# Kernel optimization log

Measured on AMD Instinct MI355X. Metric: run time of the kernel, lower is better.

Reference implementation:

```python
import jax, jax.numpy as jnp
import numpy as np

D_MODEL = 1024
N_HEAD = 16


def setup_inputs() -> dict:
    key = jax.random.key(0)
    ks = jax.random.split(key, 11)
    B, S, D = 2, 2048, D_MODEL
    s = 1.0 / np.sqrt(D)
    inp = {
        "q": jax.random.normal(ks[0], (B, S, D), jnp.float32),
        "k": jax.random.normal(ks[1], (B, S, D), jnp.float32),
        "v": jax.random.normal(ks[2], (B, S, D), jnp.float32),
        "Wq": jax.random.normal(ks[3], (D, D), jnp.float32) * s,
        "bq": jnp.zeros((D,), jnp.float32),
        "Wk": jax.random.normal(ks[4], (D, D), jnp.float32) * s,
        "bk": jnp.zeros((D,), jnp.float32),
        "Wv": jax.random.normal(ks[5], (D, D), jnp.float32) * s,
        "bv": jnp.zeros((D,), jnp.float32),
        "Wo": jax.random.normal(ks[6], (D, D), jnp.float32) * s,
        "bo": jnp.zeros((D,), jnp.float32),
    }
    return inp


def _split(x, n_head):
    B, S, D = x.shape
    return x.reshape(B, S, n_head, D // n_head).transpose(0, 2, 1, 3)  # [B,H,S,dh]


def reference(q, k, v, Wq, bq, Wk, bk, Wv, bv, Wo, bo):
    # Linear projections (torch Linear: x @ W.T + b), add_noise=False path
    qh = _split(q @ Wq.T + bq, N_HEAD)
    kh = _split(k @ Wk.T + bk, N_HEAD)
    vh = _split(v @ Wv.T + bv, N_HEAD)
    d_tensor = qh.shape[-1]
    # score = q @ k^T / sqrt(d_tensor); mask=None
    score = jnp.einsum('bhqd,bhkd->bhqk', qh, kh) / jnp.sqrt(jnp.float32(d_tensor))
    attn = jax.nn.softmax(score, axis=-1)
    out = jnp.einsum('bhqk,bhkd->bhqd', attn, vh)
    B, H, S, dh = out.shape
    out = out.transpose(0, 2, 1, 3).reshape(B, S, H * dh)
    return out @ Wo.T + bo
```

## Files before the change

kernel.cpp:

```cpp
#include <hip/hip_runtime.h>
#include <stdint.h>

typedef unsigned short u16;
typedef short bfx8 __attribute__((ext_vector_type(8)));
typedef float fx4 __attribute__((ext_vector_type(4)));

#define B_  2
#define S_  2048
#define D_  1024
#define H_  16
#define DH  64
#define K_  1024
#define M_ROWS 4096
#define QSCALE 0.18033688011112042f


__device__ __forceinline__ u16 f2bf(float x) {
  union { float f; uint32_t u; } c; c.f = x;
  uint32_t r = (c.u + 0x7FFFu + ((c.u >> 16) & 1u)) >> 16;
  return (u16)r;
}

__device__ __forceinline__ fx4 mfma16(bfx8 a, bfx8 b, fx4 c) {
  return __builtin_amdgcn_mfma_f32_16x16x32_bf16(a, b, c, 0, 0, 0);
}

typedef const __attribute__((address_space(1))) void as1_cvoid;
typedef __attribute__((address_space(3))) void as3_void;

__device__ __forceinline__ void stage16(const void* g, void* l) {
  __builtin_amdgcn_global_load_lds((as1_cvoid*)g, (as3_void*)l, 16, 0, 0);
}

__device__ __forceinline__ bfx8 lds_frag(const u16* base, int row, int kelem) {
  int off = (row << 7) + (kelem << 1);
  off ^= (row & 7) << 4;
  return *reinterpret_cast<const bfx8*>(reinterpret_cast<const char*>(base) + off);
}

__device__ __forceinline__ uint32_t cvt_pk_bf16(float lo, float hi) {
  uint32_t r;
  asm("v_cvt_pk_bf16_f32 %0, %1, %2" : "=v"(r) : "v"(lo), "v"(hi));
  return r;
}

__device__ __forceinline__ float exp2_raw(float x) {
  float r;
  asm("v_exp_f32 %0, %1" : "=v"(r) : "v"(x));
  return r;
}


__global__ __launch_bounds__(256) void convert_kernel(
    const float* __restrict__ q, const float* __restrict__ k, const float* __restrict__ v,
    const float* __restrict__ wq, const float* __restrict__ wk, const float* __restrict__ wv,
    const float* __restrict__ wo,
    u16* __restrict__ qb, u16* __restrict__ kb, u16* __restrict__ vb,
    u16* __restrict__ wqb, u16* __restrict__ wkb, u16* __restrict__ wvb,
    u16* __restrict__ wob) {
  const float* s; u16* d; int n8;
  switch (blockIdx.y) {
    case 0: s = q;  d = qb;  n8 = (M_ROWS * D_) / 8; break;
    case 1: s = k;  d = kb;  n8 = (M_ROWS * D_) / 8; break;
    case 2: s = v;  d = vb;  n8 = (M_ROWS * D_) / 8; break;
    case 3: s = wq; d = wqb; n8 = (D_ * D_) / 8; break;
    case 4: s = wk; d = wkb; n8 = (D_ * D_) / 8; break;
    case 5: s = wv; d = wvb; n8 = (D_ * D_) / 8; break;
    default: s = wo; d = wob; n8 = (D_ * D_) / 8; break;
  }
  int idx = blockIdx.x * blockDim.x + threadIdx.x;
  if (idx >= n8) return;
  const float4* sp = reinterpret_cast<const float4*>(s) + (size_t)idx * 2;
  float4 a = sp[0], b = sp[1];
  bfx8 r;
  r[0] = (short)f2bf(a.x); r[1] = (short)f2bf(a.y);
  r[2] = (short)f2bf(a.z); r[3] = (short)f2bf(a.w);
  r[4] = (short)f2bf(b.x); r[5] = (short)f2bf(b.y);
  r[6] = (short)f2bf(b.z); r[7] = (short)f2bf(b.w);
  *reinterpret_cast<bfx8*>(d + (size_t)idx * 8) = r;
}


__device__ __forceinline__ void g128_stage(const u16* __restrict__ A,
                                           const u16* __restrict__ Bt,
                                           int m0, int n0, int k0,
                                           u16* Ad, u16* Bd,
                                           int w, int l8, int c8) {
  #pragma unroll
  for (int i = 0; i < 4; ++i) {
    int j = (w << 2) + i;
    int row = (j << 3) + l8;
    int sc = c8 ^ (row & 7);
    stage16(A + (size_t)(m0 + row) * K_ + k0 + (sc << 3), Ad + (j << 9));
    stage16(Bt + (size_t)(n0 + row) * K_ + k0 + (sc << 3), Bd + (j << 9));
  }
}

__device__ __forceinline__ void gemm128_core(const u16* __restrict__ A,
                                             const u16* __restrict__ Bt,
                                             int m0, int n0,
                                             u16 (*Al)[128 * 64], u16 (*Bl)[128 * 64],
                                             fx4 (&acc)[4][4]) {
  const int lane = threadIdx.x & 63;
  const int w = threadIdx.x >> 6;
  const int l8 = lane >> 3, c8 = lane & 7;
  const int fr = lane & 15, fk = (lane >> 4) << 3;
  const int wr = (w >> 1) << 6, wc = (w & 1) << 6;

  g128_stage(A, Bt, m0, n0, 0, Al[0], Bl[0], w, l8, c8);
  __syncthreads();
  for (int t = 0; t < K_ / 64; ++t) {
    const int cur = t & 1;
    if (t + 1 < K_ / 64)
      g128_stage(A, Bt, m0, n0, (t + 1) * 64, Al[cur ^ 1], Bl[cur ^ 1], w, l8, c8);
    __builtin_amdgcn_s_setprio(1);
    #pragma unroll
    for (int kb = 0; kb < 2; ++kb) {
      bfx8 af[4], bf[4];
      #pragma unroll
      for (int rb = 0; rb < 4; ++rb)
        af[rb] = lds_frag(Al[cur], wr + rb * 16 + fr, kb * 32 + fk);
      #pragma unroll
      for (int cb = 0; cb < 4; ++cb)
        bf[cb] = lds_frag(Bl[cur], wc + cb * 16 + fr, kb * 32 + fk);
      #pragma unroll
      for (int rb = 0; rb < 4; ++rb)
        #pragma unroll
        for (int cb = 0; cb < 4; ++cb)
          acc[rb][cb] = mfma16(af[rb], bf[cb], acc[rb][cb]);
    }
    __builtin_amdgcn_s_setprio(0);
    __syncthreads();
  }
}


__global__ __launch_bounds__(256, 2) void proj_gemm(
    const u16* __restrict__ qb, const u16* __restrict__ kb, const u16* __restrict__ vb,
    const u16* __restrict__ wqb, const u16* __restrict__ wkb, const u16* __restrict__ wvb,
    const float* __restrict__ bq, const float* __restrict__ bk, const float* __restrict__ bv,
    u16* __restrict__ Qh, u16* __restrict__ Kh, u16* __restrict__ VT) {
  __shared__ alignas(16) u16 Al[2][128 * 64];
  __shared__ alignas(16) u16 Bl[2][128 * 64];
  int bid = (blockIdx.x & 7) * 96 + (blockIdx.x >> 3);
  int z = bid >> 8;
  int t = bid & 255;
  const u16 *A, *Bt; const float* bias;
  if (z == 0)      { A = qb;  Bt = wqb; bias = bq; }
  else if (z == 1) { A = kb;  Bt = wkb; bias = bk; }
  else             { A = wvb; Bt = vb;  bias = bv; }
  int m0, n0;
  if (z < 2) { m0 = (t >> 3) << 7; n0 = (t & 7) << 7; }
  else       { m0 = (t >> 5) << 7; n0 = (t & 31) << 7; }

  fx4 acc[4][4];
  #pragma unroll
  for (int i = 0; i < 4; ++i)
    #pragma unroll
    for (int j = 0; j < 4; ++j) acc[i][j] = (fx4){0.f, 0.f, 0.f, 0.f};

  gemm128_core(A, Bt, m0, n0, Al, Bl, acc);

  const int lane = threadIdx.x & 63;
  const int w = threadIdx.x >> 6;
  const int wr = (w >> 1) << 6, wc = (w & 1) << 6;
  const int fr = lane & 15;
  const int rq = (lane >> 4) << 2;

  if (z < 2) {
    u16* O = (z == 0) ? Qh : Kh;
    float scale = (z == 0) ? QSCALE : 1.0f;
    #pragma unroll
    for (int cb = 0; cb < 4; ++cb) {
      int n = n0 + wc + cb * 16 + fr;
      float bn = bias[n];
      int h = n >> 6, dd = n & 63;
      #pragma unroll
      for (int rb = 0; rb < 4; ++rb) {
        #pragma unroll
        for (int r = 0; r < 4; ++r) {
          int m = m0 + wr + rb * 16 + rq + r;
          int b = m >> 11, srow = m & 2047;
          O[((size_t)((b * H_ + h) * S_ + srow) << 6) + dd] =
              f2bf((acc[rb][cb][r] + bn) * scale);
        }
      }
    }
  } else {
    #pragma unroll
    for (int rb = 0; rb < 4; ++rb) {
      #pragma unroll
      for (int r = 0; r < 4; ++r) {
        int m = m0 + wr + rb * 16 + rq + r;
        float bm = bias[m];
        int h = m >> 6, dd = m & 63;
        #pragma unroll
        for (int cb = 0; cb < 4; ++cb) {
          int n = n0 + wc + cb * 16 + fr;
          int b = n >> 11, srow = n & 2047;
          VT[(size_t)((b * H_ + h) * DH + dd) * S_ + srow] =
              f2bf(acc[rb][cb][r] + bm);
        }
      }
    }
  }
}


__global__ __launch_bounds__(256, 2) void attn_kernel(
    const u16* __restrict__ Qh, const u16* __restrict__ Kh,
    const u16* __restrict__ VT, u16* __restrict__ AO) {
  __shared__ alignas(16) u16 Klds[2][64 * 64];
  __shared__ alignas(16) u16 Vlds[2][64 * 64];

  const int blk = ((blockIdx.x & 7) << 6) + (blockIdx.x >> 3);
  const int bh = blk >> 4;
  const int qt = blk & 15;
  const int tid = threadIdx.x;
  const int lane = tid & 63;
  const int w = tid >> 6;
  const int q0 = (qt << 7) + (w << 5);
  const int c = lane & 15;
  const int g = lane >> 4;
  const int l8 = lane >> 3;
  const int c8 = lane & 7;
  const int sc = c8 ^ l8;
  const size_t base = (size_t)bh * (S_ * DH);
  const u16* Qp = Qh + base;
  const int b = bh >> 4, h = bh & 15;

  bfx8 qf[2][2];
  #pragma unroll
  for (int rb = 0; rb < 2; ++rb)
    #pragma unroll
    for (int kbi = 0; kbi < 2; ++kbi)
      qf[rb][kbi] = *reinterpret_cast<const bfx8*>(
          Qp + (size_t)(q0 + rb * 16 + c) * DH + kbi * 32 + (g << 3));

  bfx8 ones;
  #pragma unroll
  for (int i = 0; i < 8; ++i) ones[i] = (short)0x3F80;

  fx4 acc[2][4];
  fx4 accl[2];
  #pragma unroll
  for (int rb = 0; rb < 2; ++rb) {
    accl[rb] = (fx4){0.f, 0.f, 0.f, 0.f};
    #pragma unroll
    for (int db = 0; db < 4; ++db) acc[rb][db] = (fx4){0.f, 0.f, 0.f, 0.f};
  }

  const int colA = ((g ^ (c & 3)) << 4);
  const int f6 = (c & 4) << 4;
  const int laneK = c * 128 + colA;
  const char* kb_0[2] = { (const char*)Klds[0] + laneK + f6,
                          (const char*)Klds[0] + laneK + (f6 ^ 64) };
  const char* kb_1[2] = { (const char*)Klds[1] + laneK + f6,
                          (const char*)Klds[1] + laneK + (f6 ^ 64) };
  const char* vb_0[2] = { (const char*)Vlds[0] + laneK + f6,
                          (const char*)Vlds[0] + laneK + (f6 ^ 64) };
  const char* vb_1[2] = { (const char*)Vlds[1] + laneK + f6,
                          (const char*)Vlds[1] + laneK + (f6 ^ 64) };

  const u16* kS0 = Kh + base + (size_t)((w << 4) + l8) * DH + (sc << 3);
  const u16* kS1 = kS0 + 8 * DH;
  const u16* vS0 = VT + base + (size_t)((w << 4) + l8) * S_ + (sc << 3);
  const u16* vS1 = vS0 + 8 * S_;
  u16* kD_0[2] = { &Klds[0][(2 * w) << 9], &Klds[0][(2 * w + 1) << 9] };
  u16* kD_1[2] = { &Klds[1][(2 * w) << 9], &Klds[1][(2 * w + 1) << 9] };
  u16* vD_0[2] = { &Vlds[0][(2 * w) << 9], &Vlds[0][(2 * w + 1) << 9] };
  u16* vD_1[2] = { &Vlds[1][(2 * w) << 9], &Vlds[1][(2 * w + 1) << 9] };

#define STAGEB(bi)                                                            \
  do {                                                                        \
    stage16(kS0, kD_##bi[0]); stage16(kS1, kD_##bi[1]);                       \
    stage16(vS0, vD_##bi[0]); stage16(vS1, vD_##bi[1]);                       \
    kS0 += 64 * DH; kS1 += 64 * DH; vS0 += 64; vS1 += 64;                     \
  } while (0)

#define COMPUTE(bi)                                                           \
  do {                                                                        \
    fx4 sf[2][4];                                                             \
    _Pragma("unroll") for (int rb = 0; rb < 2; ++rb)                          \
      _Pragma("unroll") for (int cb = 0; cb < 4; ++cb)                        \
        sf[rb][cb] = (fx4){0.f, 0.f, 0.f, 0.f};                               \
    __builtin_amdgcn_s_setprio(1);                                            \
    _Pragma("unroll") for (int kbi = 0; kbi < 2; ++kbi) {                     \
      bfx8 kf[4];                                                             \
      _Pragma("unroll") for (int cb = 0; cb < 4; ++cb)                        \
        kf[cb] = *reinterpret_cast<const bfx8*>(kb_##bi[kbi] + cb * 2048);    \
      _Pragma("unroll") for (int rb = 0; rb < 2; ++rb)                        \
        _Pragma("unroll") for (int cb = 0; cb < 4; ++cb)                      \
          sf[rb][cb] = mfma16(kf[cb], qf[rb][kbi], sf[rb][cb]);               \
    }                                                                         \
    __builtin_amdgcn_s_setprio(0);                                            \
    uint32_t E[2][2][2][2];                                                   \
    _Pragma("unroll") for (int rb = 0; rb < 2; ++rb) {                        \
      _Pragma("unroll") for (int cb = 0; cb < 4; ++cb)                        \
        _Pragma("unroll") for (int r = 0; r < 4; ++r)                         \
          sf[rb][cb][r] = exp2_raw(sf[rb][cb][r]);                            \
      _Pragma("unroll") for (int cb = 0; cb < 4; ++cb)                        \
        _Pragma("unroll") for (int hh = 0; hh < 2; ++hh)                      \
          E[rb][cb >> 1][cb & 1][hh] =                                        \
              cvt_pk_bf16(sf[rb][cb][2 * hh], sf[rb][cb][2 * hh + 1]);        \
      _Pragma("unroll") for (int r2 = 0; r2 < 2; ++r2)                        \
        _Pragma("unroll") for (int r0 = 0; r0 < 2; ++r0) {                    \
          asm("v_permlane32_swap_b32 %0, %1"                                  \
              : "+v"(E[rb][r2][0][r0]), "+v"(E[rb][r2][1][r0]));              \
          asm("v_permlane16_swap_b32 %0, %1"                                  \
              : "+v"(E[rb][r2][0][r0]), "+v"(E[rb][r2][1][r0]));              \
        }                                                                     \
    }                                                                         \
    __builtin_amdgcn_s_setprio(1);                                            \
    _Pragma("unroll") for (int kbi = 0; kbi < 2; ++kbi) {                     \
      bfx8 vf[4];                                                             \
      _Pragma("unroll") for (int db = 0; db < 4; ++db)                        \
        vf[db] = *reinterpret_cast<const bfx8*>(vb_##bi[kbi] + db * 2048);    \
      _Pragma("unroll") for (int rb = 0; rb < 2; ++rb) {                      \
        union { uint32_t wd[4]; bfx8 v; } pu;                                 \
        pu.wd[0] = E[rb][kbi][0][0]; pu.wd[1] = E[rb][kbi][0][1];             \
        pu.wd[2] = E[rb][kbi][1][0]; pu.wd[3] = E[rb][kbi][1][1];             \
        _Pragma("unroll") for (int db = 0; db < 4; ++db)                      \
          acc[rb][db] = mfma16(pu.v, vf[db], acc[rb][db]);                    \
        accl[rb] = mfma16(pu.v, ones, accl[rb]);                              \
      }                                                                       \
    }                                                                         \
    __builtin_amdgcn_s_setprio(0);                                            \
  } while (0)

  STAGEB(0);
  __syncthreads();

  for (int kv = 0; kv < S_; kv += 128) {
    STAGEB(1);
    COMPUTE(0);
    __syncthreads();
    if (kv + 128 < S_) STAGEB(0);
    COMPUTE(1);
    __syncthreads();
  }
#undef STAGEB
#undef COMPUTE

  #pragma unroll
  for (int rb = 0; rb < 2; ++rb) {
    float invb[4];
    #pragma unroll
    for (int r = 0; r < 4; ++r) invb[r] = 1.0f / accl[rb][r];
    #pragma unroll
    for (int db = 0; db < 4; ++db)
      #pragma unroll
      for (int r = 0; r < 4; ++r) {
        int qrow = q0 + rb * 16 + (g << 2) + r;
        AO[(size_t)(b * S_ + qrow) * D_ + h * DH + db * 16 + c] =
            f2bf(acc[rb][db][r] * invb[r]);
      }
  }
}


__global__ __launch_bounds__(256, 2) void out_gemm(
    const u16* __restrict__ AO, const u16* __restrict__ wob,
    const float* __restrict__ bo, float* __restrict__ out) {
  __shared__ alignas(16) u16 Al[2][128 * 64];
  __shared__ alignas(16) u16 Bl[2][128 * 64];
  int t = (blockIdx.x & 7) * 32 + (blockIdx.x >> 3);
  int m0 = (t >> 3) << 7, n0 = (t & 7) << 7;
  fx4 acc[4][4];
  #pragma unroll
  for (int i = 0; i < 4; ++i)
    #pragma unroll
    for (int j = 0; j < 4; ++j) acc[i][j] = (fx4){0.f, 0.f, 0.f, 0.f};
  gemm128_core(AO, wob, m0, n0, Al, Bl, acc);
  const int lane = threadIdx.x & 63;
  const int w = threadIdx.x >> 6;
  const int wr = (w >> 1) << 6, wc = (w & 1) << 6;
  #pragma unroll
  for (int cb = 0; cb < 4; ++cb) {
    int n = n0 + wc + cb * 16 + (lane & 15);
    float bn = bo[n];
    #pragma unroll
    for (int rb = 0; rb < 4; ++rb)
      #pragma unroll
      for (int r = 0; r < 4; ++r) {
        int m = m0 + wr + rb * 16 + ((lane >> 4) << 2) + r;
        out[(size_t)m * D_ + n] = acc[rb][cb][r] + bn;
      }
  }
}


extern "C" void kernel_launch(void* const* d_in, const int* in_sizes, int n_in,
                              void* d_out, int out_size, void* d_ws, size_t ws_size,
                              hipStream_t stream) {
  (void)in_sizes; (void)n_in; (void)out_size;
  const size_t MB = 1024 * 1024;
  if (ws_size < 56 * MB) return;

  const float* q  = (const float*)d_in[0];
  const float* k  = (const float*)d_in[1];
  const float* v  = (const float*)d_in[2];
  const float* Wq = (const float*)d_in[3];
  const float* bq = (const float*)d_in[4];
  const float* Wk = (const float*)d_in[5];
  const float* bk = (const float*)d_in[6];
  const float* Wv = (const float*)d_in[7];
  const float* bv = (const float*)d_in[8];
  const float* Wo = (const float*)d_in[9];
  const float* bo = (const float*)d_in[10];
  float* out = (float*)d_out;

  char* ws = (char*)d_ws;
  u16* qb  = (u16*)(ws);
  u16* kb  = (u16*)(ws + 8 * MB);
  u16* vb  = (u16*)(ws + 16 * MB);
  u16* wqb = (u16*)(ws + 24 * MB);
  u16* wkb = (u16*)(ws + 26 * MB);
  u16* wvb = (u16*)(ws + 28 * MB);
  u16* wob = (u16*)(ws + 30 * MB);
  u16* Qh  = (u16*)(ws + 32 * MB);
  u16* Kh  = (u16*)(ws + 40 * MB);
  u16* VT  = (u16*)(ws + 48 * MB);
  u16* AO  = qb;

  convert_kernel<<<dim3(2048, 7), 256, 0, stream>>>(q, k, v, Wq, Wk, Wv, Wo,
                                                    qb, kb, vb, wqb, wkb, wvb, wob);
  proj_gemm<<<768, 256, 0, stream>>>(qb, kb, vb, wqb, wkb, wvb, bq, bk, bv, Qh, Kh, VT);
  attn_kernel<<<512, 256, 0, stream>>>(Qh, Kh, VT, AO);
  out_gemm<<<256, 256, 0, stream>>>(AO, wob, bo, out);
}
```

Measured before the change: 214.5 us.

## Fuse fp32-to-bf16 conversion into GEMM tile loading and drop convert kernel

Removes the separate conversion kernel. The projection and output GEMMs now load fp32 inputs and weights straight from global memory into registers, convert them to bf16 with packed converts, and write them into swizzled LDS double buffers. This saves one launch and a full write-then-reread of bf16 copies. In exchange, each GEMM tile reloads twice as many bytes of fp32 data, and weights are converted again by every block that reads them. Register-staged prefetch replaces the async LDS staging for those operands.

Measured after the change: 232.4 us. +8.3%, slower.

```diff
diff --git a/kernel.cpp b/kernel.cpp
--- a/kernel.cpp
+++ b/kernel.cpp
@@ -50,94 +50,58 @@
   return r;
 }
 
-
-__global__ __launch_bounds__(256) void convert_kernel(
-    const float* __restrict__ q, const float* __restrict__ k, const float* __restrict__ v,
-    const float* __restrict__ wq, const float* __restrict__ wk, const float* __restrict__ wv,
-    const float* __restrict__ wo,
-    u16* __restrict__ qb, u16* __restrict__ kb, u16* __restrict__ vb,
-    u16* __restrict__ wqb, u16* __restrict__ wkb, u16* __restrict__ wvb,
-    u16* __restrict__ wob) {
-  const float* s; u16* d; int n8;
-  switch (blockIdx.y) {
-    case 0: s = q;  d = qb;  n8 = (M_ROWS * D_) / 8; break;
-    case 1: s = k;  d = kb;  n8 = (M_ROWS * D_) / 8; break;
-    case 2: s = v;  d = vb;  n8 = (M_ROWS * D_) / 8; break;
-    case 3: s = wq; d = wqb; n8 = (D_ * D_) / 8; break;
-    case 4: s = wk; d = wkb; n8 = (D_ * D_) / 8; break;
-    case 5: s = wv; d = wvb; n8 = (D_ * D_) / 8; break;
-    default: s = wo; d = wob; n8 = (D_ * D_) / 8; break;
-  }
-  int idx = blockIdx.x * blockDim.x + threadIdx.x;
-  if (idx >= n8) return;
-  const float4* sp = reinterpret_cast<const float4*>(s) + (size_t)idx * 2;
-  float4 a = sp[0], b = sp[1];
-  bfx8 r;
-  r[0] = (short)f2bf(a.x); r[1] = (short)f2bf(a.y);
-  r[2] = (short)f2bf(a.z); r[3] = (short)f2bf(a.w);
-  r[4] = (short)f2bf(b.x); r[5] = (short)f2bf(b.y);
-  r[6] = (short)f2bf(b.z); r[7] = (short)f2bf(b.w);
-  *reinterpret_cast<bfx8*>(d + (size_t)idx * 8) = r;
-}
-
-
-__device__ __forceinline__ void g128_stage(const u16* __restrict__ A,
-                                           const u16* __restrict__ Bt,
-                                           int m0, int n0, int k0,
-                                           u16* Ad, u16* Bd,
-                                           int w, int l8, int c8) {
+struct f32x8 { float4 a, b; };
+__device__ __forceinline__ f32x8 ld8(const float* p) {
+  const float4* p4 = reinterpret_cast<const float4*>(p);
+  f32x8 r; r.a = p4[0]; r.b = p4[1]; return r;
+}
+__device__ __forceinline__ void wr8(u16* d, f32x8 v) {
+  union { uint32_t w[4]; bfx8 x; } u;
+  u.w[0] = cvt_pk_bf16(v.a.x, v.a.y);
+  u.w[1] = cvt_pk_bf16(v.a.z, v.a.w);
+  u.w[2] = cvt_pk_bf16(v.b.x, v.b.y);
+  u.w[3] = cvt_pk_bf16(v.b.z, v.b.w);
+  *reinterpret_cast<bfx8*>(d) = u.x;
+}
+
+__device__ __forceinline__ void g128_stageA(const u16* __restrict__ A,
+                                            int m0, int k0, u16* Ad,
+                                            int w, int l8, int c8) {
   #pragma unroll
   for (int i = 0; i < 4; ++i) {
     int j = (w << 2) + i;
     int row = (j << 3) + l8;
     int sc = c8 ^ (row & 7);
     stage16(A + (size_t)(m0 + row) * K_ + k0 + (sc << 3), Ad + (j << 9));
-    stage16(Bt + (size_t)(n0 + row) * K_ + k0 + (sc << 3), Bd + (j << 9));
-  }
-}
-
-__device__ __forceinline__ void gemm128_core(const u16* __restrict__ A,
-                                             const u16* __restrict__ Bt,
-                                             int m0, int n0,
-                                             u16 (*Al)[128 * 64], u16 (*Bl)[128 * 64],
-                                             fx4 (&acc)[4][4]) {
-  const int lane = threadIdx.x & 63;
-  const int w = threadIdx.x >> 6;
-  const int l8 = lane >> 3, c8 = lane & 7;
-  const int fr = lane & 15, fk = (lane >> 4) << 3;
-  const int wr = (w >> 1) << 6, wc = (w & 1) << 6;
-
-  g128_stage(A, Bt, m0, n0, 0, Al[0], Bl[0], w, l8, c8);
-  __syncthreads();
-  for (int t = 0; t < K_ / 64; ++t) {
-    const int cur = t & 1;
-    if (t + 1 < K_ / 64)
-      g128_stage(A, Bt, m0, n0, (t + 1) * 64, Al[cur ^ 1], Bl[cur ^ 1], w, l8, c8);
-    __builtin_amdgcn_s_setprio(1);
-    #pragma unroll
-    for (int kb = 0; kb < 2; ++kb) {
-      bfx8 af[4], bf[4];
-      #pragma unroll
-      for (int rb = 0; rb < 4; ++rb)
-        af[rb] = lds_frag(Al[cur], wr + rb * 16 + fr, kb * 32 + fk);
+  }
+}
+
+__device__ __forceinline__ void mfma_block(const u16* Ac, const u16* Bc,
+                                           int wr, int wc, int fr, int fk,
+                                           fx4 (&acc)[4][4]) {
+  __builtin_amdgcn_s_setprio(1);
+  #pragma unroll
+  for (int kb = 0; kb < 2; ++kb) {
+    bfx8 af[4], bf[4];
+    #pragma unroll
+    for (int rb = 0; rb < 4; ++rb)
+      af[rb] = lds_frag(Ac, wr + rb * 16 + fr, kb * 32 + fk);
+    #pragma unroll
+    for (int cb = 0; cb < 4; ++cb)
+      bf[cb] = lds_frag(Bc, wc + cb * 16 + fr, kb * 32 + fk);
+    #pragma unroll
+    for (int rb = 0; rb < 4; ++rb)
       #pragma unroll
       for (int cb = 0; cb < 4; ++cb)
-        bf[cb] = lds_frag(Bl[cur], wc + cb * 16 + fr, kb * 32 + fk);
-      #pragma unroll
-      for (int rb = 0; rb < 4; ++rb)
-        #pragma unroll
-        for (int cb = 0; cb < 4; ++cb)
-          acc[rb][cb] = mfma16(af[rb], bf[cb], acc[rb][cb]);
-    }
-    __builtin_amdgcn_s_setprio(0);
-    __syncthreads();
-  }
+        acc[rb][cb] = mfma16(af[rb], bf[cb], acc[rb][cb]);
+  }
+  __builtin_amdgcn_s_setprio(0);
 }
 
 
 __global__ __launch_bounds__(256, 2) void proj_gemm(
-    const u16* __restrict__ qb, const u16* __restrict__ kb, const u16* __restrict__ vb,
-    const u16* __restrict__ wqb, const u16* __restrict__ wkb, const u16* __restrict__ wvb,
+    const float* __restrict__ q, const float* __restrict__ k, const float* __restrict__ v,
+    const float* __restrict__ Wq, const float* __restrict__ Wk, const float* __restrict__ Wv,
     const float* __restrict__ bq, const float* __restrict__ bk, const float* __restrict__ bv,
     u16* __restrict__ Qh, u16* __restrict__ Kh, u16* __restrict__ VT) {
   __shared__ alignas(16) u16 Al[2][128 * 64];
@@ -145,28 +109,67 @@
   int bid = (blockIdx.x & 7) * 96 + (blockIdx.x >> 3);
   int z = bid >> 8;
   int t = bid & 255;
-  const u16 *A, *Bt; const float* bias;
-  if (z == 0)      { A = qb;  Bt = wqb; bias = bq; }
-  else if (z == 1) { A = kb;  Bt = wkb; bias = bk; }
-  else             { A = wvb; Bt = vb;  bias = bv; }
+  const float *A, *Bt; const float* bias;
+  if (z == 0)      { A = q;  Bt = Wq; bias = bq; }
+  else if (z == 1) { A = k;  Bt = Wk; bias = bk; }
+  else             { A = Wv; Bt = v;  bias = bv; }
   int m0, n0;
   if (z < 2) { m0 = (t >> 3) << 7; n0 = (t & 7) << 7; }
   else       { m0 = (t >> 5) << 7; n0 = (t & 31) << 7; }
 
-  fx4 acc[4][4];
-  #pragma unroll
-  for (int i = 0; i < 4; ++i)
-    #pragma unroll
-    for (int j = 0; j < 4; ++j) acc[i][j] = (fx4){0.f, 0.f, 0.f, 0.f};
-
-  gemm128_core(A, Bt, m0, n0, Al, Bl, acc);
-
   const int lane = threadIdx.x & 63;
   const int w = threadIdx.x >> 6;
+  const int l8 = lane >> 3, c8 = lane & 7;
+  const int fr = lane & 15, fk = (lane >> 4) << 3;
   const int wr = (w >> 1) << 6, wc = (w & 1) << 6;
-  const int fr = lane & 15;
+
+  const float* As[4]; const float* Bs[4]; int doff[4];
+  #pragma unroll
+  for (int i = 0; i < 4; ++i) {
+    int j = (w << 2) + i, row = (j << 3) + l8, sc = c8 ^ (row & 7);
+    As[i] = A + (size_t)(m0 + row) * K_ + (sc << 3);
+    Bs[i] = Bt + (size_t)(n0 + row) * K_ + (sc << 3);
+    doff[i] = (j << 9) + (lane << 3);
+  }
+
+  fx4 acc[4][4];
+  #pragma unroll
+  for (int i = 0; i < 4; ++i)
+    #pragma unroll
+    for (int j = 0; j < 4; ++j) acc[i][j] = (fx4){0.f, 0.f, 0.f, 0.f};
+
+  f32x8 ra[4], rb[4];
+  #pragma unroll
+  for (int i = 0; i < 4; ++i) {
+    ra[i] = ld8(As[i]); rb[i] = ld8(Bs[i]);
+    As[i] += 64; Bs[i] += 64;
+  }
+  #pragma unroll
+  for (int i = 0; i < 4; ++i) {
+    wr8(&Al[0][doff[i]], ra[i]); wr8(&Bl[0][doff[i]], rb[i]);
+  }
+  __syncthreads();
+
+  for (int tt = 0; tt < 16; ++tt) {
+    const int cur = tt & 1;
+    if (tt < 15) {
+      #pragma unroll
+      for (int i = 0; i < 4; ++i) {
+        ra[i] = ld8(As[i]); rb[i] = ld8(Bs[i]);
+        As[i] += 64; Bs[i] += 64;
+      }
+    }
+    mfma_block(Al[cur], Bl[cur], wr, wc, fr, fk, acc);
+    if (tt < 15) {
+      #pragma unroll
+      for (int i = 0; i < 4; ++i) {
+        wr8(&Al[cur ^ 1][doff[i]], ra[i]); wr8(&Bl[cur ^ 1][doff[i]], rb[i]);
+      }
+    }
+    __syncthreads();
+  }
+
   const int rq = (lane >> 4) << 2;
-
   if (z < 2) {
     u16* O = (z == 0) ? Qh : Kh;
     float scale = (z == 0) ? QSCALE : 1.0f;
@@ -176,22 +179,22 @@
       float bn = bias[n];
       int h = n >> 6, dd = n & 63;
       #pragma unroll
-      for (int rb = 0; rb < 4; ++rb) {
+      for (int rb_ = 0; rb_ < 4; ++rb_) {
         #pragma unroll
         for (int r = 0; r < 4; ++r) {
-          int m = m0 + wr + rb * 16 + rq + r;
+          int m = m0 + wr + rb_ * 16 + rq + r;
           int b = m >> 11, srow = m & 2047;
           O[((size_t)((b * H_ + h) * S_ + srow) << 6) + dd] =
-              f2bf((acc[rb][cb][r] + bn) * scale);
+              f2bf((acc[rb_][cb][r] + bn) * scale);
         }
       }
     }
   } else {
     #pragma unroll
-    for (int rb = 0; rb < 4; ++rb) {
+    for (int rb_ = 0; rb_ < 4; ++rb_) {
       #pragma unroll
       for (int r = 0; r < 4; ++r) {
-        int m = m0 + wr + rb * 16 + rq + r;
+        int m = m0 + wr + rb_ * 16 + rq + r;
         float bm = bias[m];
         int h = m >> 6, dd = m & 63;
         #pragma unroll
@@ -199,7 +202,7 @@
           int n = n0 + wc + cb * 16 + fr;
           int b = n >> 11, srow = n & 2047;
           VT[(size_t)((b * H_ + h) * DH + dd) * S_ + srow] =
-              f2bf(acc[rb][cb][r] + bm);
+              f2bf(acc[rb_][cb][r] + bm);
         }
       }
     }
@@ -360,31 +363,66 @@
 
 
 __global__ __launch_bounds__(256, 2) void out_gemm(
-    const u16* __restrict__ AO, const u16* __restrict__ wob,
+    const u16* __restrict__ AO, const float* __restrict__ Wo,
     const float* __restrict__ bo, float* __restrict__ out) {
   __shared__ alignas(16) u16 Al[2][128 * 64];
   __shared__ alignas(16) u16 Bl[2][128 * 64];
   int t = (blockIdx.x & 7) * 32 + (blockIdx.x >> 3);
   int m0 = (t >> 3) << 7, n0 = (t & 7) << 7;
-  fx4 acc[4][4];
-  #pragma unroll
-  for (int i = 0; i < 4; ++i)
-    #pragma unroll
-    for (int j = 0; j < 4; ++j) acc[i][j] = (fx4){0.f, 0.f, 0.f, 0.f};
-  gemm128_core(AO, wob, m0, n0, Al, Bl, acc);
+
   const int lane = threadIdx.x & 63;
   const int w = threadIdx.x >> 6;
+  const int l8 = lane >> 3, c8 = lane & 7;
+  const int fr = lane & 15, fk = (lane >> 4) << 3;
   const int wr = (w >> 1) << 6, wc = (w & 1) << 6;
+
+  const float* Bs[4]; int doff[4];
+  #pragma unroll
+  for (int i = 0; i < 4; ++i) {
+    int j = (w << 2) + i, row = (j << 3) + l8, sc = c8 ^ (row & 7);
+    Bs[i] = Wo + (size_t)(n0 + row) * K_ + (sc << 3);
+    doff[i] = (j << 9) + (lane << 3);
+  }
+
+  fx4 acc[4][4];
+  #pragma unroll
+  for (int i = 0; i < 4; ++i)
+    #pragma unroll
+    for (int j = 0; j < 4; ++j) acc[i][j] = (fx4){0.f, 0.f, 0.f, 0.f};
+
+  f32x8 rb[4];
+  #pragma unroll
+  for (int i = 0; i < 4; ++i) { rb[i] = ld8(Bs[i]); Bs[i] += 64; }
+  #pragma unroll
+  for (int i = 0; i < 4; ++i) wr8(&Bl[0][doff[i]], rb[i]);
+  g128_stageA(AO, m0, 0, Al[0], w, l8, c8);
+  __syncthreads();
+
+  for (int tt = 0; tt < 16; ++tt) {
+    const int cur = tt & 1;
+    if (tt < 15) {
+      g128_stageA(AO, m0, (tt + 1) * 64, Al[cur ^ 1], w, l8, c8);
+      #pragma unroll
+      for (int i = 0; i < 4; ++i) { rb[i] = ld8(Bs[i]); Bs[i] += 64; }
+    }
+    mfma_block(Al[cur], Bl[cur], wr, wc, fr, fk, acc);
+    if (tt < 15) {
+      #pragma unroll
+      for (int i = 0; i < 4; ++i) wr8(&Bl[cur ^ 1][doff[i]], rb[i]);
+    }
+    __syncthreads();
+  }
+
   #pragma unroll
   for (int cb = 0; cb < 4; ++cb) {
-    int n = n0 + wc + cb * 16 + (lane & 15);
+    int n = n0 + wc + cb * 16 + fr;
     float bn = bo[n];
     #pragma unroll
-    for (int rb = 0; rb < 4; ++rb)
+    for (int rb_ = 0; rb_ < 4; ++rb_)
       #pragma unroll
       for (int r = 0; r < 4; ++r) {
-        int m = m0 + wr + rb * 16 + ((lane >> 4) << 2) + r;
-        out[(size_t)m * D_ + n] = acc[rb][cb][r] + bn;
+        int m = m0 + wr + rb_ * 16 + ((lane >> 4) << 2) + r;
+        out[(size_t)m * D_ + n] = acc[rb_][cb][r] + bn;
       }
   }
 }
@@ -395,7 +433,7 @@
                               hipStream_t stream) {
   (void)in_sizes; (void)n_in; (void)out_size;
   const size_t MB = 1024 * 1024;
-  if (ws_size < 56 * MB) return;
+  if (ws_size < 32 * MB) return;
 
   const float* q  = (const float*)d_in[0];
   const float* k  = (const float*)d_in[1];
@@ -411,21 +449,12 @@
   float* out = (float*)d_out;
 
   char* ws = (char*)d_ws;
-  u16* qb  = (u16*)(ws);
-  u16* kb  = (u16*)(ws + 8 * MB);
-  u16* vb  = (u16*)(ws + 16 * MB);
-  u16* wqb = (u16*)(ws + 24 * MB);
-  u16* wkb = (u16*)(ws + 26 * MB);
-  u16* wvb = (u16*)(ws + 28 * MB);
-  u16* wob = (u16*)(ws + 30 * MB);
-  u16* Qh  = (u16*)(ws + 32 * MB);
-  u16* Kh  = (u16*)(ws + 40 * MB);
-  u16* VT  = (u16*)(ws + 48 * MB);
-  u16* AO  = qb;
-
-  convert_kernel<<<dim3(2048, 7), 256, 0, stream>>>(q, k, v, Wq, Wk, Wv, Wo,
-                                                    qb, kb, vb, wqb, wkb, wvb, wob);
-  proj_gemm<<<768, 256, 0, stream>>>(qb, kb, vb, wqb, wkb, wvb, bq, bk, bv, Qh, Kh, VT);
+  u16* Qh = (u16*)(ws);
+  u16* Kh = (u16*)(ws + 8 * MB);
+  u16* VT = (u16*)(ws + 16 * MB);
+  u16* AO = (u16*)(ws + 24 * MB);
+
+  proj_gemm<<<768, 256, 0, stream>>>(q, k, v, Wq, Wk, Wv, bq, bk, bv, Qh, Kh, VT);
   attn_kernel<<<512, 256, 0, stream>>>(Qh, Kh, VT, AO);
-  out_gemm<<<256, 256, 0, stream>>>(AO, wob, bo, out);
-}
+  out_gemm<<<256, 256, 0, stream>>>(AO, Wo, bo, out);
+}
```

## Split attention KV range across two wave groups and halve out-GEMM tile width

Applied to the files above, without the earlier changes.

The attention kernel now launches 512 threads per block. Two groups of four waves each process half of the key/value sequence with their own LDS double buffers, and the partial accumulators and row sums are merged through shared memory before normalisation. This doubles the wave count per query tile to hide latency and improve occupancy, at the cost of a final LDS reduction and a larger shared-memory footprint. The output GEMM switches to 128x64 tiles with 512 blocks and an inline staging loop, giving better fill across CUs with less B reuse per block.

New measurement: 209.7 us. 1.02x faster.

```diff
diff --git a/kernel.cpp b/kernel.cpp
--- a/kernel.cpp
+++ b/kernel.cpp
@@ -207,11 +207,10 @@
 }
 
 
-__global__ __launch_bounds__(256, 2) void attn_kernel(
+__global__ __launch_bounds__(512, 4) void attn_kernel(
     const u16* __restrict__ Qh, const u16* __restrict__ Kh,
     const u16* __restrict__ VT, u16* __restrict__ AO) {
-  __shared__ alignas(16) u16 Klds[2][64 * 64];
-  __shared__ alignas(16) u16 Vlds[2][64 * 64];
+  __shared__ alignas(16) u16 SH[2][2][2][64 * 64];
 
   const int blk = ((blockIdx.x & 7) << 6) + (blockIdx.x >> 3);
   const int bh = blk >> 4;
@@ -219,7 +218,9 @@
   const int tid = threadIdx.x;
   const int lane = tid & 63;
   const int w = tid >> 6;
-  const int q0 = (qt << 7) + (w << 5);
+  const int grp = w >> 2;
+  const int wl = w & 3;
+  const int q0 = (qt << 7) + (wl << 5);
   const int c = lane & 15;
   const int g = lane >> 4;
   const int l8 = lane >> 3;
@@ -253,23 +254,23 @@
   const int colA = ((g ^ (c & 3)) << 4);
   const int f6 = (c & 4) << 4;
   const int laneK = c * 128 + colA;
-  const char* kb_0[2] = { (const char*)Klds[0] + laneK + f6,
-                          (const char*)Klds[0] + laneK + (f6 ^ 64) };
-  const char* kb_1[2] = { (const char*)Klds[1] + laneK + f6,
-                          (const char*)Klds[1] + laneK + (f6 ^ 64) };
-  const char* vb_0[2] = { (const char*)Vlds[0] + laneK + f6,
-                          (const char*)Vlds[0] + laneK + (f6 ^ 64) };
-  const char* vb_1[2] = { (const char*)Vlds[1] + laneK + f6,
-                          (const char*)Vlds[1] + laneK + (f6 ^ 64) };
-
-  const u16* kS0 = Kh + base + (size_t)((w << 4) + l8) * DH + (sc << 3);
+  const char* kb_0[2] = { (const char*)&SH[grp][0][0][0] + laneK + f6,
+                          (const char*)&SH[grp][0][0][0] + laneK + (f6 ^ 64) };
+  const char* kb_1[2] = { (const char*)&SH[grp][1][0][0] + laneK + f6,
+                          (const char*)&SH[grp][1][0][0] + laneK + (f6 ^ 64) };
+  const char* vb_0[2] = { (const char*)&SH[grp][0][1][0] + laneK + f6,
+                          (const char*)&SH[grp][0][1][0] + laneK + (f6 ^ 64) };
+  const char* vb_1[2] = { (const char*)&SH[grp][1][1][0] + laneK + f6,
+                          (const char*)&SH[grp][1][1][0] + laneK + (f6 ^ 64) };
+
+  const u16* kS0 = Kh + base + (size_t)(grp * 1024 + (wl << 4) + l8) * DH + (sc << 3);
   const u16* kS1 = kS0 + 8 * DH;
-  const u16* vS0 = VT + base + (size_t)((w << 4) + l8) * S_ + (sc << 3);
+  const u16* vS0 = VT + base + (size_t)((wl << 4) + l8) * S_ + grp * 1024 + (sc << 3);
   const u16* vS1 = vS0 + 8 * S_;
-  u16* kD_0[2] = { &Klds[0][(2 * w) << 9], &Klds[0][(2 * w + 1) << 9] };
-  u16* kD_1[2] = { &Klds[1][(2 * w) << 9], &Klds[1][(2 * w + 1) << 9] };
-  u16* vD_0[2] = { &Vlds[0][(2 * w) << 9], &Vlds[0][(2 * w + 1) << 9] };
-  u16* vD_1[2] = { &Vlds[1][(2 * w) << 9], &Vlds[1][(2 * w + 1) << 9] };
+  u16* kD_0[2] = { &SH[grp][0][0][(2 * wl) << 9], &SH[grp][0][0][(2 * wl + 1) << 9] };
+  u16* kD_1[2] = { &SH[grp][1][0][(2 * wl) << 9], &SH[grp][1][0][(2 * wl + 1) << 9] };
+  u16* vD_0[2] = { &SH[grp][0][1][(2 * wl) << 9], &SH[grp][0][1][(2 * wl + 1) << 9] };
+  u16* vD_1[2] = { &SH[grp][1][1][(2 * wl) << 9], &SH[grp][1][1][(2 * wl + 1) << 9] };
 
 #define STAGEB(bi)                                                            \
   do {                                                                        \
@@ -331,30 +332,59 @@
   STAGEB(0);
   __syncthreads();
 
-  for (int kv = 0; kv < S_; kv += 128) {
+  for (int t = 0; t < 16; t += 2) {
     STAGEB(1);
     COMPUTE(0);
     __syncthreads();
-    if (kv + 128 < S_) STAGEB(0);
+    if (t + 2 < 16) STAGEB(0);
     COMPUTE(1);
     __syncthreads();
   }
 #undef STAGEB
 #undef COMPUTE
 
-  #pragma unroll
-  for (int rb = 0; rb < 2; ++rb) {
-    float invb[4];
-    #pragma unroll
-    for (int r = 0; r < 4; ++r) invb[r] = 1.0f / accl[rb][r];
-    #pragma unroll
-    for (int db = 0; db < 4; ++db)
-      #pragma unroll
-      for (int r = 0; r < 4; ++r) {
-        int qrow = q0 + rb * 16 + (g << 2) + r;
-        AO[(size_t)(b * S_ + qrow) * D_ + h * DH + db * 16 + c] =
-            f2bf(acc[rb][db][r] * invb[r]);
-      }
+  float* MG = (float*)&SH[0][0][0][0];
+  const int sl = (wl << 6) + lane;
+  if (w >= 4) {
+    #pragma unroll
+    for (int rb = 0; rb < 2; ++rb) {
+      #pragma unroll
+      for (int db = 0; db < 4; ++db)
+        #pragma unroll
+        for (int r = 0; r < 4; ++r)
+          MG[(rb * 16 + db * 4 + r) * 256 + sl] = acc[rb][db][r];
+      #pragma unroll
+      for (int r = 0; r < 4; ++r)
+        MG[(32 + rb * 4 + r) * 256 + sl] = accl[rb][r];
+    }
+  }
+  __syncthreads();
+  if (w < 4) {
+    #pragma unroll
+    for (int rb = 0; rb < 2; ++rb) {
+      #pragma unroll
+      for (int db = 0; db < 4; ++db)
+        #pragma unroll
+        for (int r = 0; r < 4; ++r)
+          acc[rb][db][r] += MG[(rb * 16 + db * 4 + r) * 256 + sl];
+      #pragma unroll
+      for (int r = 0; r < 4; ++r)
+        accl[rb][r] += MG[(32 + rb * 4 + r) * 256 + sl];
+    }
+    #pragma unroll
+    for (int rb = 0; rb < 2; ++rb) {
+      float invb[4];
+      #pragma unroll
+      for (int r = 0; r < 4; ++r) invb[r] = 1.0f / accl[rb][r];
+      #pragma unroll
+      for (int db = 0; db < 4; ++db)
+        #pragma unroll
+        for (int r = 0; r < 4; ++r) {
+          int qrow = q0 + rb * 16 + (g << 2) + r;
+          AO[(size_t)(b * S_ + qrow) * D_ + h * DH + db * 16 + c] =
+              f2bf(acc[rb][db][r] * invb[r]);
+        }
+    }
   }
 }
 
@@ -363,21 +393,74 @@
     const u16* __restrict__ AO, const u16* __restrict__ wob,
     const float* __restrict__ bo, float* __restrict__ out) {
   __shared__ alignas(16) u16 Al[2][128 * 64];
-  __shared__ alignas(16) u16 Bl[2][128 * 64];
-  int t = (blockIdx.x & 7) * 32 + (blockIdx.x >> 3);
-  int m0 = (t >> 3) << 7, n0 = (t & 7) << 7;
-  fx4 acc[4][4];
-  #pragma unroll
-  for (int i = 0; i < 4; ++i)
-    #pragma unroll
-    for (int j = 0; j < 4; ++j) acc[i][j] = (fx4){0.f, 0.f, 0.f, 0.f};
-  gemm128_core(AO, wob, m0, n0, Al, Bl, acc);
+  __shared__ alignas(16) u16 Bl[2][64 * 64];
+  int t = (blockIdx.x & 7) * 64 + (blockIdx.x >> 3);
+  int m0 = (t >> 4) << 7, n0 = (t & 15) << 6;
+
   const int lane = threadIdx.x & 63;
   const int w = threadIdx.x >> 6;
-  const int wr = (w >> 1) << 6, wc = (w & 1) << 6;
-  #pragma unroll
-  for (int cb = 0; cb < 4; ++cb) {
-    int n = n0 + wc + cb * 16 + (lane & 15);
+  const int l8 = lane >> 3, c8 = lane & 7;
+  const int fr = lane & 15, fk = (lane >> 4) << 3;
+  const int wr = (w >> 1) << 6, wc = (w & 1) << 5;
+
+#define OSTAGE(buf, k0)                                                       \
+  do {                                                                        \
+    _Pragma("unroll")                                                         \
+    for (int i = 0; i < 4; ++i) {                                             \
+      int j = (w << 2) + i;                                                   \
+      int row = (j << 3) + l8;                                                \
+      int scx = c8 ^ (row & 7);                                               \
+      stage16(AO + (size_t)(m0 + row) * K_ + (k0) + (scx << 3),               \
+              Al[buf] + (j << 9));                                            \
+    }                                                                         \
+    _Pragma("unroll")                                                         \
+    for (int i = 0; i < 2; ++i) {                                             \
+      int j = (w << 1) + i;                                                   \
+      int row = (j << 3) + l8;                                                \
+      int scx = c8 ^ (row & 7);                                               \
+      stage16(wob + (size_t)(n0 + row) * K_ + (k0) + (scx << 3),              \
+              Bl[buf] + (j << 9));                                            \
+    }                                                                         \
+  } while (0)
+
+  fx4 acc[4][2];
+  #pragma unroll
+  for (int i = 0; i < 4; ++i)
+    #pragma unroll
+    for (int j = 0; j < 2; ++j) acc[i][j] = (fx4){0.f, 0.f, 0.f, 0.f};
+
+  OSTAGE(0, 0);
+  __syncthreads();
+  for (int tt = 0; tt < 16; ++tt) {
+    const int cur = tt & 1;
+    if (tt < 15) {
+      if (cur == 0) OSTAGE(1, (tt + 1) * 64);
+      else          OSTAGE(0, (tt + 1) * 64);
+    }
+    __builtin_amdgcn_s_setprio(1);
+    #pragma unroll
+    for (int kb = 0; kb < 2; ++kb) {
+      bfx8 af[4], bf[2];
+      #pragma unroll
+      for (int rb = 0; rb < 4; ++rb)
+        af[rb] = lds_frag(Al[cur], wr + rb * 16 + fr, kb * 32 + fk);
+      #pragma unroll
+      for (int cb = 0; cb < 2; ++cb)
+        bf[cb] = lds_frag(Bl[cur], wc + cb * 16 + fr, kb * 32 + fk);
+      #pragma unroll
+      for (int rb = 0; rb < 4; ++rb)
+        #pragma unroll
+        for (int cb = 0; cb < 2; ++cb)
+          acc[rb][cb] = mfma16(af[rb], bf[cb], acc[rb][cb]);
+    }
+    __builtin_amdgcn_s_setprio(0);
+    __syncthreads();
+  }
+#undef OSTAGE
+
+  #pragma unroll
+  for (int cb = 0; cb < 2; ++cb) {
+    int n = n0 + wc + cb * 16 + fr;
     float bn = bo[n];
     #pragma unroll
     for (int rb = 0; rb < 4; ++rb)
@@ -426,6 +509,6 @@
   convert_kernel<<<dim3(2048, 7), 256, 0, stream>>>(q, k, v, Wq, Wk, Wv, Wo,
                                                     qb, kb, vb, wqb, wkb, wvb, wob);
   proj_gemm<<<768, 256, 0, stream>>>(qb, kb, vb, wqb, wkb, wvb, bq, bk, bv, Qh, Kh, VT);
-  attn_kernel<<<512, 256, 0, stream>>>(Qh, Kh, VT, AO);
-  out_gemm<<<256, 256, 0, stream>>>(AO, wob, bo, out);
-}
+  attn_kernel<<<512, 512, 0, stream>>>(Qh, Kh, VT, AO);
+  out_gemm<<<512, 256, 0, stream>>>(AO, wob, bo, out);
+}
```
